# Kernel optimization log

Hardware: AMD Instinct MI355X
Metric: run time of the kernel (lower is better)

Reference implementation:

```python
import jax, jax.numpy as jnp
import numpy as np

K = 3          # kernel_size
STRIDE_H = 1
STRIDE_W = 1


def setup_inputs() -> dict:
    key = jax.random.key(0)
    k1, k2, k3, k4 = jax.random.split(key, 4)
    inputs = jax.random.normal(k1, (8, 128, 128, 128), dtype=jnp.float32)
    weight = jax.random.normal(k2, (128, 128, K, K), dtype=jnp.float32) * 0.05
    # learned per-image rate map, fractional dilations in [1, 3)
    rates = jax.random.uniform(k3, (1, 1, 32, 32), dtype=jnp.float32) * 2.0 + 1.0
    bias = jax.random.normal(k4, (128,), dtype=jnp.float32) * 0.01
    return {"inputs": inputs, "weight": weight, "rates": rates, "bias": bias}


def _interp_bilinear(r, out_h, out_w):
    # torch F.interpolate(mode='bilinear', align_corners=False) on a 2D map r[in_h,in_w]
    in_h, in_w = r.shape
    def src(n_out, n_in):
        s = (jnp.arange(n_out, dtype=jnp.float32) + 0.5) * (n_in / n_out) - 0.5
        return jnp.clip(s, 0.0, n_in - 1.0)
    sy = src(out_h, in_h)
    sx = src(out_w, in_w)
    y0 = jnp.floor(sy).astype(jnp.int32)
    x0 = jnp.floor(sx).astype(jnp.int32)
    y1 = jnp.minimum(y0 + 1, in_h - 1)
    x1 = jnp.minimum(x0 + 1, in_w - 1)
    wy = (sy - y0.astype(jnp.float32))[:, None]   # [out_h,1]
    wx = (sx - x0.astype(jnp.float32))[None, :]   # [1,out_w]
    return (r[y0[:, None], x0[None, :]] * (1 - wy) * (1 - wx)
            + r[y0[:, None], x1[None, :]] * (1 - wy) * wx
            + r[y1[:, None], x0[None, :]] * wy * (1 - wx)
            + r[y1[:, None], x1[None, :]] * wy * wx)


def _bilinear_sample(img, y, x):
    # img: [N,C,H,W]; y,x: [Ho,Wo] float positions; zero padding outside.
    H, W = img.shape[2], img.shape[3]
    y0 = jnp.floor(y).astype(jnp.int32)
    x0 = jnp.floor(x).astype(jnp.int32)
    y1, x1 = y0 + 1, x0 + 1
    wy = y - y0.astype(img.dtype)
    wx = x - x0.astype(img.dtype)
    def tap(yi, xi):
        m = ((yi >= 0) & (yi < H) & (xi >= 0) & (xi < W)).astype(img.dtype)
        yc = jnp.clip(yi, 0, H - 1)
        xc = jnp.clip(xi, 0, W - 1)
        return img[:, :, yc, xc] * m  # [N,C,Ho,Wo]
    return (tap(y0, x0) * (1 - wy) * (1 - wx)
            + tap(y0, x1) * (1 - wy) * wx
            + tap(y1, x0) * wy * (1 - wx)
            + tap(y1, x1) * wy * wx)


def reference(inputs, weight, rates, bias):
    N, Cin, H, W = inputs.shape
    Ho = (H - K) // STRIDE_H + 1
    Wo = (W - K) // STRIDE_W + 1
    rate = _interp_bilinear(rates[0, 0], Ho, Wo)          # [Ho,Wo]
    base_y = jnp.arange(Ho, dtype=jnp.float32)[:, None] * STRIDE_H
    base_x = jnp.arange(Wo, dtype=jnp.float32)[None, :] * STRIDE_W
    out = jnp.broadcast_to(bias[None, :, None, None], (N, weight.shape[0], Ho, Wo)).astype(inputs.dtype)
    # fixed K*K = 9 taps; each tap samples the input at p0 + k*rate (per-pixel dilation)
    for kh in range(K):
        for kw in range(K):
            y = base_y + kh * rate
            x = base_x + kw * rate
            samp = _bilinear_sample(inputs, y, x)          # [N,Cin,Ho,Wo]
            out = out + jnp.einsum('oc,nchw->nohw', weight[:, :, kh, kw], samp)
    return out
```

## Files before the change

### kernel.cpp

```cpp
#include <hip/hip_runtime.h>
#include <hip/hip_fp16.h>

#define N_    8
#define CIN   128
#define COUT  128
#define H_    128
#define W_    128
#define HO    126
#define WO    126
#define PIXPER (HO*WO)
#define TOTPIX (N_*PIXPER)
#define PT    128
#define BLKPERIMG 125
#define NBLK  (N_*BLKPERIMG)
#define SSTR  136

typedef _Float16 f16x8 __attribute__((ext_vector_type(8)));
typedef _Float16 f16x4 __attribute__((ext_vector_type(4)));
typedef float    f32x4 __attribute__((ext_vector_type(4)));

union U4H {
    uint4   u;
    __half2 h[4];
    f16x8   f;
};

__global__ __launch_bounds__(256) void transpose_in_kernel(
    const float* __restrict__ in, _Float16* __restrict__ in_cl)
{
    __shared__ float tile[64][65];
    int bid = blockIdx.x;
    int hwt = bid & 255;
    int ct  = (bid >> 8) & 1;
    int n   = bid >> 9;
    int r0  = threadIdx.x >> 4;
    int c4  = (threadIdx.x & 15) * 4;
    const float* src = in + ((size_t)(n * CIN + ct * 64) * 16384) + hwt * 64;
#pragma unroll
    for (int k = 0; k < 4; ++k) {
        int row = r0 + k * 16;
        float4 v = *(const float4*)(src + (size_t)row * 16384 + c4);
        *(float4*)&tile[row][c4] = v;
    }
    __syncthreads();
    _Float16* dst = in_cl + ((size_t)(n * 16384 + hwt * 64) * 128) + ct * 64;
#pragma unroll
    for (int k = 0; k < 4; ++k) {
        int hw = r0 + k * 16;
        f16x4 o;
        o[0] = (_Float16)tile[c4 + 0][hw];
        o[1] = (_Float16)tile[c4 + 1][hw];
        o[2] = (_Float16)tile[c4 + 2][hw];
        o[3] = (_Float16)tile[c4 + 3][hw];
        *(f16x4*)(dst + (size_t)hw * 128 + c4) = o;
    }
}

__global__ void transpose_w_kernel(const float* __restrict__ w, _Float16* __restrict__ wt) {
    int t = blockIdx.x * 256 + threadIdx.x;
    int o = t >> 7, c = t & 127;
    const float* s = w + (size_t)(o * 128 + c) * 9;
#pragma unroll
    for (int tap = 0; tap < 9; ++tap)
        wt[tap * 16384 + o * 128 + c] = (_Float16)s[tap];
}

__global__ __launch_bounds__(256, 2) void adc_main(
    const _Float16* __restrict__ in_cl, const _Float16* __restrict__ wt,
    const float* __restrict__ rates, const float* __restrict__ bias,
    float* __restrict__ out)
{
    __shared__ uint4    sW[2048];
    __shared__ __align__(16) _Float16 sS[PT * SSTR];
    __shared__ int      sPYi[3][PT];
    __shared__ float    sPYf[3][PT];
    __shared__ int      sPXi[3][PT];
    __shared__ float    sPXf[3][PT];

    const int t    = threadIdx.x;
    const int lane = t & 63;
    const int wv   = t >> 6;
    const int l15  = lane & 15;
    const int quad = lane >> 4;

    const int n     = blockIdx.x & 7;
    const int pbase = (blockIdx.x >> 3) * PT;

    if (t < PT) {
        int rem = min(pbase + t, PIXPER - 1);
        int ho = rem / WO, wo = rem - ho * WO;
        const float sc = 32.0f / 126.0f;
        float sy = fminf(fmaxf(((float)ho + 0.5f) * sc - 0.5f, 0.0f), 31.0f);
        float sx = fminf(fmaxf(((float)wo + 0.5f) * sc - 0.5f, 0.0f), 31.0f);
        int y0 = (int)sy, x0 = (int)sx;
        int y1 = min(y0 + 1, 31), x1 = min(x0 + 1, 31);
        float wy = sy - (float)y0, wx = sx - (float)x0;
        float r = rates[y0 * 32 + x0] * (1.0f - wy) * (1.0f - wx)
                + rates[y0 * 32 + x1] * (1.0f - wy) * wx
                + rates[y1 * 32 + x0] * wy * (1.0f - wx)
                + rates[y1 * 32 + x1] * wy * wx;
#pragma unroll
        for (int k = 0; k < 3; ++k) {
            float fy  = (float)ho + (float)k * r;
            float fy0 = floorf(fy);
            sPYi[k][t] = (int)fy0;
            sPYf[k][t] = fy - fy0;
            float fx  = (float)wo + (float)k * r;
            float fx0 = floorf(fx);
            sPXi[k][t] = (int)fx0;
            sPXf[k][t] = fx - fx0;
        }
    }

    f32x4 acc[8][2];
    const f32x4 zero = {0.0f, 0.0f, 0.0f, 0.0f};
#pragma unroll
    for (int i = 0; i < 8; ++i) { acc[i][0] = zero; acc[i][1] = zero; }

    __syncthreads();

    const int grp = t >> 4;
    const int gl  = t & 15;
    const unsigned nbase = (unsigned)n << 14;

#pragma unroll
    for (int tap = 0; tap < 9; ++tap) {
        const int kh = tap / 3;
        const int kw = tap - kh * 3;

        const uint4* wsrc = (const uint4*)(wt + tap * 16384);
#pragma unroll
        for (int i = 0; i < 8; ++i) {
            int gi = i * 256 + t;
            int o = gi >> 4, g = gi & 15;
            sW[(o << 4) | (g ^ (o & 7))] = wsrc[gi];
        }

#pragma unroll
        for (int j = 0; j < 8; ++j) {
            int px = grp * 8 + j;
            int   y0 = sPYi[kh][px];  float wy = sPYf[kh][px];
            int   x0 = sPXi[kw][px];  float wx = sPXf[kw][px];
            int yc0 = min(y0, H_ - 1), yc1 = min(y0 + 1, H_ - 1);
            int xc0 = min(x0, W_ - 1), xc1 = min(x0 + 1, W_ - 1);
            unsigned lo = (unsigned)(gl * 8);
            U4H A, B, C, D, S;
            A.u = *(const uint4*)(in_cl + (((nbase + (unsigned)(yc0 * W_ + xc0)) << 7) + lo));
            if (kw != 0) B.u = *(const uint4*)(in_cl + (((nbase + (unsigned)(yc0 * W_ + xc1)) << 7) + lo));
            if (kh != 0) C.u = *(const uint4*)(in_cl + (((nbase + (unsigned)(yc1 * W_ + xc0)) << 7) + lo));
            if (kh != 0 && kw != 0)
                         D.u = *(const uint4*)(in_cl + (((nbase + (unsigned)(yc1 * W_ + xc1)) << 7) + lo));
            if (kh == 0 && kw == 0) {
                S.u = A.u;
            } else {
                float vy0 = (y0 <= H_ - 1) ? 1.0f : 0.0f;
                float vy1 = (y0 <= H_ - 2) ? 1.0f : 0.0f;
                float vx0 = (x0 <= W_ - 1) ? 1.0f : 0.0f;
                float vx1 = (x0 <= W_ - 2) ? 1.0f : 0.0f;
                __half2 w00v = __float2half2_rn((1.0f - wy) * (1.0f - wx) * vy0 * vx0);
                __half2 w01v = __float2half2_rn((1.0f - wy) * wx * vy0 * vx1);
                __half2 w10v = __float2half2_rn(wy * (1.0f - wx) * vy1 * vx0);
                __half2 w11v = __float2half2_rn(wy * wx * vy1 * vx1);
#pragma unroll
                for (int d = 0; d < 4; ++d) {
                    __half2 s = __hmul2(A.h[d], w00v);
                    if (kw != 0)            s = __hfma2(B.h[d], w01v, s);
                    if (kh != 0)            s = __hfma2(C.h[d], w10v, s);
                    if (kh != 0 && kw != 0) s = __hfma2(D.h[d], w11v, s);
                    S.h[d] = s;
                }
            }
            *(f16x8*)&sS[px * SSTR + gl * 8] = S.f;
        }
        __syncthreads();

#pragma unroll
        for (int ks = 0; ks < 4; ++ks) {
            f16x8 b0 = *(const f16x8*)&sS[(wv * 32 +      l15) * SSTR + ks * 32 + quad * 8];
            f16x8 b1 = *(const f16x8*)&sS[(wv * 32 + 16 + l15) * SSTR + ks * 32 + quad * 8];
#pragma unroll
            for (int mt = 0; mt < 8; ++mt) {
                int o = (mt << 4) | l15;
                int g = (ks << 2) | quad;
                U4H AF;
                AF.u = sW[(o << 4) | (g ^ (o & 7))];
                acc[mt][0] = __builtin_amdgcn_mfma_f32_16x16x32_f16(AF.f, b0, acc[mt][0], 0, 0, 0);
                acc[mt][1] = __builtin_amdgcn_mfma_f32_16x16x32_f16(AF.f, b1, acc[mt][1], 0, 0, 0);
            }
        }
        __syncthreads();
    }

#pragma unroll
    for (int pt = 0; pt < 2; ++pt) {
        int p    = (wv << 5) + (pt << 4) + l15;
        int prel = pbase + p;
        int rem2 = min(prel, PIXPER - 1);
        float* obase = out + (size_t)n * (COUT * PIXPER) + rem2;
        if (prel < PIXPER) {
#pragma unroll
            for (int mt = 0; mt < 8; ++mt) {
                int o0 = (mt << 4) + (quad << 2);
                float4 bs = *(const float4*)(bias + o0);
                f32x4 a0 = acc[mt][pt];
                obase[(size_t)(o0 + 0) * PIXPER] = a0[0] + bs.x;
                obase[(size_t)(o0 + 1) * PIXPER] = a0[1] + bs.y;
                obase[(size_t)(o0 + 2) * PIXPER] = a0[2] + bs.z;
                obase[(size_t)(o0 + 3) * PIXPER] = a0[3] + bs.w;
            }
        }
    }
}

extern "C" void kernel_launch(void* const* d_in, const int* in_sizes, int n_in,
                              void* d_out, int out_size, void* d_ws, size_t ws_size,
                              hipStream_t stream) {
    const float* inputs = (const float*)d_in[0];
    const float* weight = (const float*)d_in[1];
    const float* rates  = (const float*)d_in[2];
    const float* bias   = (const float*)d_in[3];
    float* out = (float*)d_out;

    char* ws = (char*)d_ws;
    _Float16* in_cl = (_Float16*)ws;
    _Float16* wtp   = (_Float16*)(ws + 33554432);

    transpose_w_kernel<<<64, 256, 0, stream>>>(weight, wtp);
    transpose_in_kernel<<<4096, 256, 0, stream>>>(inputs, in_cl);
    adc_main<<<NBLK, 256, 0, stream>>>(in_cl, wtp, rates, bias, out);
}
```

Baseline: 189.6 us.

## Pre-swizzle weights into MFMA fragment layout, load from global; precompute tap offsets

The weight pre-transpose now writes weights directly in the per-lane MFMA fragment order, so the main kernel reads A fragments straight from global memory instead of staging them in shared memory each tap. This frees LDS and drops a per-tap copy, which allows launch bounds to request 3 blocks per CU. Per-pixel row/column base offsets and masked half-precision interpolation factors are precomputed into packed shared arrays, which reduces index arithmetic in the gather loop. The input transpose is retiled to 32 channels by 128 pixels with wider fp16 stores. The trade-off is repeated global/L2 weight reads per block in place of LDS reuse.

```diff
diff --git a/kernel.cpp b/kernel.cpp
--- a/kernel.cpp
+++ b/kernel.cpp
@@ -28,54 +28,54 @@
 __global__ __launch_bounds__(256) void transpose_in_kernel(
     const float* __restrict__ in, _Float16* __restrict__ in_cl)
 {
-    __shared__ float tile[64][65];
+    __shared__ float tile[32][129];
     int bid = blockIdx.x;
-    int hwt = bid & 255;
-    int ct  = (bid >> 8) & 1;
+    int hwt = bid & 127;
+    int ct  = (bid >> 7) & 3;
     int n   = bid >> 9;
-    int r0  = threadIdx.x >> 4;
-    int c4  = (threadIdx.x & 15) * 4;
-    const float* src = in + ((size_t)(n * CIN + ct * 64) * 16384) + hwt * 64;
-#pragma unroll
-    for (int k = 0; k < 4; ++k) {
-        int row = r0 + k * 16;
-        float4 v = *(const float4*)(src + (size_t)row * 16384 + c4);
-        *(float4*)&tile[row][c4] = v;
+    int t   = threadIdx.x;
+
+    int f4 = t & 31;
+    const float* src = in + ((size_t)(n * CIN + ct * 32) * 16384) + hwt * 128;
+#pragma unroll
+    for (int i = 0; i < 4; ++i) {
+        int c = (t >> 5) + i * 8;
+        float4 v = *(const float4*)(src + (size_t)c * 16384 + f4 * 4);
+        *(float4*)&tile[c][f4 * 4] = v;
     }
     __syncthreads();
-    _Float16* dst = in_cl + ((size_t)(n * 16384 + hwt * 64) * 128) + ct * 64;
-#pragma unroll
-    for (int k = 0; k < 4; ++k) {
-        int hw = r0 + k * 16;
-        f16x4 o;
-        o[0] = (_Float16)tile[c4 + 0][hw];
-        o[1] = (_Float16)tile[c4 + 1][hw];
-        o[2] = (_Float16)tile[c4 + 2][hw];
-        o[3] = (_Float16)tile[c4 + 3][hw];
-        *(f16x4*)(dst + (size_t)hw * 128 + c4) = o;
-    }
-}
-
-__global__ void transpose_w_kernel(const float* __restrict__ w, _Float16* __restrict__ wt) {
+    int hw  = t >> 1;
+    int c16 = (t & 1) * 16;
+    _Float16* dst = in_cl + ((size_t)(n * 16384 + hwt * 128 + hw) * 128) + ct * 32 + c16;
+    f16x8 lo, hi;
+#pragma unroll
+    for (int j = 0; j < 8; ++j) lo[j] = (_Float16)tile[c16 + j][hw];
+#pragma unroll
+    for (int j = 0; j < 8; ++j) hi[j] = (_Float16)tile[c16 + 8 + j][hw];
+    *(f16x8*)dst       = lo;
+    *(f16x8*)(dst + 8) = hi;
+}
+
+__global__ void transpose_w_kernel(const float* __restrict__ w, _Float16* __restrict__ wt2) {
     int t = blockIdx.x * 256 + threadIdx.x;
     int o = t >> 7, c = t & 127;
+    int mt = o >> 4, l15 = o & 15;
+    int ks = c >> 5, quad = (c >> 3) & 3, d = c & 7;
+    int lane = quad * 16 + l15;
     const float* s = w + (size_t)(o * 128 + c) * 9;
 #pragma unroll
     for (int tap = 0; tap < 9; ++tap)
-        wt[tap * 16384 + o * 128 + c] = (_Float16)s[tap];
-}
-
-__global__ __launch_bounds__(256, 2) void adc_main(
-    const _Float16* __restrict__ in_cl, const _Float16* __restrict__ wt,
+        wt2[(size_t)((tap * 8 + mt) * 4 + ks) * 512 + lane * 8 + d] = (_Float16)s[tap];
+}
+
+__global__ __launch_bounds__(256, 3) void adc_main(
+    const _Float16* __restrict__ in_cl, const _Float16* __restrict__ wt2,
     const float* __restrict__ rates, const float* __restrict__ bias,
     float* __restrict__ out)
 {
-    __shared__ uint4    sW[2048];
     __shared__ __align__(16) _Float16 sS[PT * SSTR];
-    __shared__ int      sPYi[3][PT];
-    __shared__ float    sPYf[3][PT];
-    __shared__ int      sPXi[3][PT];
-    __shared__ float    sPXf[3][PT];
+    __shared__ uint4 sKH[3 * PT];
+    __shared__ uint4 sKW[3 * PT];
 
     const int t    = threadIdx.x;
     const int lane = t & 63;
@@ -85,6 +85,7 @@
 
     const int n     = blockIdx.x & 7;
     const int pbase = (blockIdx.x >> 3) * PT;
+    const unsigned nbase = (unsigned)n << 14;
 
     if (t < PT) {
         int rem = min(pbase + t, PIXPER - 1);
@@ -92,23 +93,41 @@
         const float sc = 32.0f / 126.0f;
         float sy = fminf(fmaxf(((float)ho + 0.5f) * sc - 0.5f, 0.0f), 31.0f);
         float sx = fminf(fmaxf(((float)wo + 0.5f) * sc - 0.5f, 0.0f), 31.0f);
-        int y0 = (int)sy, x0 = (int)sx;
-        int y1 = min(y0 + 1, 31), x1 = min(x0 + 1, 31);
-        float wy = sy - (float)y0, wx = sx - (float)x0;
-        float r = rates[y0 * 32 + x0] * (1.0f - wy) * (1.0f - wx)
-                + rates[y0 * 32 + x1] * (1.0f - wy) * wx
-                + rates[y1 * 32 + x0] * wy * (1.0f - wx)
-                + rates[y1 * 32 + x1] * wy * wx;
+        int ry0 = (int)sy, rx0 = (int)sx;
+        int ry1 = min(ry0 + 1, 31), rx1 = min(rx0 + 1, 31);
+        float rwy = sy - (float)ry0, rwx = sx - (float)rx0;
+        float r = rates[ry0 * 32 + rx0] * (1.0f - rwy) * (1.0f - rwx)
+                + rates[ry0 * 32 + rx1] * (1.0f - rwy) * rwx
+                + rates[ry1 * 32 + rx0] * rwy * (1.0f - rwx)
+                + rates[ry1 * 32 + rx1] * rwy * rwx;
 #pragma unroll
         for (int k = 0; k < 3; ++k) {
             float fy  = (float)ho + (float)k * r;
-            float fy0 = floorf(fy);
-            sPYi[k][t] = (int)fy0;
-            sPYf[k][t] = fy - fy0;
+            float y0f = floorf(fy);
+            int   y0  = (int)y0f;
+            float wy  = fy - y0f;
+            float a0  = (y0 <= H_ - 1) ? (1.0f - wy) : 0.0f;
+            float a1  = (y0 <= H_ - 2) ? wy : 0.0f;
+            int yc0 = min(y0, H_ - 1), yc1 = min(y0 + 1, H_ - 1);
+            uint4 P;
+            P.x = (nbase + (unsigned)(yc0 * W_)) << 7;
+            P.y = (nbase + (unsigned)(yc1 * W_)) << 7;
+            P.z = __builtin_bit_cast(unsigned, __float2half2_rn(a0));
+            P.w = __builtin_bit_cast(unsigned, __float2half2_rn(a1));
+            sKH[k * PT + t] = P;
             float fx  = (float)wo + (float)k * r;
-            float fx0 = floorf(fx);
-            sPXi[k][t] = (int)fx0;
-            sPXf[k][t] = fx - fx0;
+            float x0f = floorf(fx);
+            int   x0  = (int)x0f;
+            float wx  = fx - x0f;
+            float b0  = (x0 <= W_ - 1) ? (1.0f - wx) : 0.0f;
+            float b1  = (x0 <= W_ - 2) ? wx : 0.0f;
+            int xc0 = min(x0, W_ - 1), xc1 = min(x0 + 1, W_ - 1);
+            uint4 Q;
+            Q.x = (unsigned)xc0 << 7;
+            Q.y = (unsigned)xc1 << 7;
+            Q.z = __builtin_bit_cast(unsigned, __float2half2_rn(b0));
+            Q.w = __builtin_bit_cast(unsigned, __float2half2_rn(b1));
+            sKW[k * PT + t] = Q;
         }
     }
 
@@ -121,46 +140,35 @@
 
     const int grp = t >> 4;
     const int gl  = t & 15;
-    const unsigned nbase = (unsigned)n << 14;
+    const unsigned lo = (unsigned)(gl * 8);
 
 #pragma unroll
     for (int tap = 0; tap < 9; ++tap) {
         const int kh = tap / 3;
         const int kw = tap - kh * 3;
 
-        const uint4* wsrc = (const uint4*)(wt + tap * 16384);
-#pragma unroll
-        for (int i = 0; i < 8; ++i) {
-            int gi = i * 256 + t;
-            int o = gi >> 4, g = gi & 15;
-            sW[(o << 4) | (g ^ (o & 7))] = wsrc[gi];
-        }
-
 #pragma unroll
         for (int j = 0; j < 8; ++j) {
             int px = grp * 8 + j;
-            int   y0 = sPYi[kh][px];  float wy = sPYf[kh][px];
-            int   x0 = sPXi[kw][px];  float wx = sPXf[kw][px];
-            int yc0 = min(y0, H_ - 1), yc1 = min(y0 + 1, H_ - 1);
-            int xc0 = min(x0, W_ - 1), xc1 = min(x0 + 1, W_ - 1);
-            unsigned lo = (unsigned)(gl * 8);
+            uint4 P = sKH[kh * PT + px];
+            uint4 Q = sKW[kw * PT + px];
+            unsigned aA = P.x + Q.x + lo;
             U4H A, B, C, D, S;
-            A.u = *(const uint4*)(in_cl + (((nbase + (unsigned)(yc0 * W_ + xc0)) << 7) + lo));
-            if (kw != 0) B.u = *(const uint4*)(in_cl + (((nbase + (unsigned)(yc0 * W_ + xc1)) << 7) + lo));
-            if (kh != 0) C.u = *(const uint4*)(in_cl + (((nbase + (unsigned)(yc1 * W_ + xc0)) << 7) + lo));
-            if (kh != 0 && kw != 0)
-                         D.u = *(const uint4*)(in_cl + (((nbase + (unsigned)(yc1 * W_ + xc1)) << 7) + lo));
+            A.u = *(const uint4*)(in_cl + aA);
+            if (kw != 0) B.u = *(const uint4*)(in_cl + (P.x + Q.y + lo));
+            if (kh != 0) C.u = *(const uint4*)(in_cl + (P.y + Q.x + lo));
+            if (kh != 0 && kw != 0) D.u = *(const uint4*)(in_cl + (P.y + Q.y + lo));
             if (kh == 0 && kw == 0) {
                 S.u = A.u;
             } else {
-                float vy0 = (y0 <= H_ - 1) ? 1.0f : 0.0f;
-                float vy1 = (y0 <= H_ - 2) ? 1.0f : 0.0f;
-                float vx0 = (x0 <= W_ - 1) ? 1.0f : 0.0f;
-                float vx1 = (x0 <= W_ - 2) ? 1.0f : 0.0f;
-                __half2 w00v = __float2half2_rn((1.0f - wy) * (1.0f - wx) * vy0 * vx0);
-                __half2 w01v = __float2half2_rn((1.0f - wy) * wx * vy0 * vx1);
-                __half2 w10v = __float2half2_rn(wy * (1.0f - wx) * vy1 * vx0);
-                __half2 w11v = __float2half2_rn(wy * wx * vy1 * vx1);
+                __half2 a0h = __builtin_bit_cast(__half2, P.z);
+                __half2 a1h = __builtin_bit_cast(__half2, P.w);
+                __half2 b0h = __builtin_bit_cast(__half2, Q.z);
+                __half2 b1h = __builtin_bit_cast(__half2, Q.w);
+                __half2 w00v = __hmul2(a0h, b0h);
+                __half2 w01v = (kw != 0) ? __hmul2(a0h, b1h) : __half2{};
+                __half2 w10v = (kh != 0) ? __hmul2(a1h, b0h) : __half2{};
+                __half2 w11v = (kh != 0 && kw != 0) ? __hmul2(a1h, b1h) : __half2{};
 #pragma unroll
                 for (int d = 0; d < 4; ++d) {
                     __half2 s = __hmul2(A.h[d], w00v);
@@ -174,18 +182,16 @@
         }
         __syncthreads();
 
+        const _Float16* wbase = wt2 + (size_t)tap * 16384 + lane * 8;
 #pragma unroll
         for (int ks = 0; ks < 4; ++ks) {
             f16x8 b0 = *(const f16x8*)&sS[(wv * 32 +      l15) * SSTR + ks * 32 + quad * 8];
             f16x8 b1 = *(const f16x8*)&sS[(wv * 32 + 16 + l15) * SSTR + ks * 32 + quad * 8];
 #pragma unroll
             for (int mt = 0; mt < 8; ++mt) {
-                int o = (mt << 4) | l15;
-                int g = (ks << 2) | quad;
-                U4H AF;
-                AF.u = sW[(o << 4) | (g ^ (o & 7))];
-                acc[mt][0] = __builtin_amdgcn_mfma_f32_16x16x32_f16(AF.f, b0, acc[mt][0], 0, 0, 0);
-                acc[mt][1] = __builtin_amdgcn_mfma_f32_16x16x32_f16(AF.f, b1, acc[mt][1], 0, 0, 0);
+                f16x8 af = *(const f16x8*)(wbase + (mt * 4 + ks) * 512);
+                acc[mt][0] = __builtin_amdgcn_mfma_f32_16x16x32_f16(af, b0, acc[mt][0], 0, 0, 0);
+                acc[mt][1] = __builtin_amdgcn_mfma_f32_16x16x32_f16(af, b1, acc[mt][1], 0, 0, 0);
             }
         }
         __syncthreads();
@@ -223,9 +229,9 @@
 
     char* ws = (char*)d_ws;
     _Float16* in_cl = (_Float16*)ws;
-    _Float16* wtp   = (_Float16*)(ws + 33554432);
-
-    transpose_w_kernel<<<64, 256, 0, stream>>>(weight, wtp);
+    _Float16* wt2   = (_Float16*)(ws + 33554432);
+
+    transpose_w_kernel<<<64, 256, 0, stream>>>(weight, wt2);
     transpose_in_kernel<<<4096, 256, 0, stream>>>(inputs, in_cl);
-    adc_main<<<NBLK, 256, 0, stream>>>(in_cl, wtp, rates, bias, out);
-}
+    adc_main<<<NBLK, 256, 0, stream>>>(in_cl, wt2, rates, bias, out);
+}
```

After: 223.5 us. +17.9%, slower.
